# Optimization experiments

Hardware: AMD Instinct MI355X
Metric: run time of the kernel (lower is better)

## Reference

```python
import jax, jax.numpy as jnp
import numpy as np

B, L, DIM, HEADS = 4, 1024, 512, 8
HD = DIM // HEADS
HID = max(64, DIM // 2)
WIN = 32
SPARSITY = 0.3
TEMP = 1.0
PAT_TAU = 0.5


def setup_inputs() -> dict:
    key = jax.random.key(0)
    ks = jax.random.split(key, 8)
    gn = lambda k, shape, sc: jax.random.normal(k, shape, jnp.float32) * sc
    return {
        "x": jax.random.normal(ks[0], (B, L, DIM), jnp.float32),
        "mask": jnp.ones((B, L), jnp.int32),
        "Wqkv": gn(ks[1], (3 * DIM, DIM), 0.02),
        "Wproj": gn(ks[2], (DIM, DIM), 0.02),
        "bproj": jnp.zeros((DIM,), jnp.float32),
        "Wsel1": gn(ks[3], (HID, DIM), 0.05),
        "bsel1": jnp.zeros((HID,), jnp.float32),
        "Wsel2": gn(ks[4], (3, HID), 0.05),
        "bsel2": jnp.zeros((3,), jnp.float32),
        "log_pattern_tau": jnp.asarray(np.log(PAT_TAU), jnp.float32),
        "sparse_w": gn(ks[5], (HEADS,), 0.2),
        "sparse_b": jnp.zeros((HEADS,), jnp.float32),
    }


def reference(x, mask, Wqkv, Wproj, bproj, Wsel1, bsel1, Wsel2, bsel2,
              log_pattern_tau, sparse_w, sparse_b):
    Bq, Lq, D = x.shape
    scale = HD ** -0.5
    qkv = (x @ Wqkv.T).reshape(Bq, Lq, 3, HEADS, HD)
    q = jnp.transpose(qkv[:, :, 0], (0, 2, 1, 3))  # (B,H,L,hd)
    k = jnp.transpose(qkv[:, :, 1], (0, 2, 1, 3))
    v = jnp.transpose(qkv[:, :, 2], (0, 2, 1, 3))
    scores = jnp.einsum('bhid,bhjd->bhij', q, k) * scale  # (B,H,L,L)

    # pattern selector on mean-pooled features (eval: no gumbel, no dropout)
    pooled = x.mean(axis=1)
    logits = jax.nn.relu(pooled @ Wsel1.T + bsel1) @ Wsel2.T + bsel2  # (B,3)
    tau = jnp.clip(jnp.exp(log_pattern_tau), 1e-4, 10.0)
    pw = jax.nn.softmax(logits / tau, axis=-1)  # (B,3)

    half = WIN // 2
    ii = jnp.arange(Lq)[:, None]
    jj = jnp.arange(Lq)[None, :]
    local = ((jj >= ii - half) & (jj <= ii + half)).astype(jnp.float32)

    # learned sparse top-k mask per head via kth-value threshold
    kk = max(1, int(Lq * (1.0 - SPARSITY)))
    s = scores * sparse_w[None, :, None, None] + sparse_b[None, :, None, None]
    kth = jax.lax.top_k(s, kk)[0][..., -1:]
    smask = (s >= kth).astype(jnp.float32)  # (B,H,L,L)

    combined = (pw[:, 0, None, None, None] * local[None, None]
                + pw[:, 1, None, None, None]
                + pw[:, 2, None, None, None] * smask)
    neg = jnp.float32(-1e9)
    scores = jnp.where(combined > 0.05, scores, neg)
    scores = jnp.where(mask[:, None, None, :] == 0, neg, scores)

    # fallback: if a row is fully masked, unmask position 0
    all_masked = jnp.all(scores <= neg + 1e-6, axis=-1)  # (B,H,L)
    scores = scores.at[..., 0].set(jnp.where(all_masked, 0.0, scores[..., 0]))

    attn = jax.nn.softmax(scores / TEMP, axis=-1)
    out = jnp.einsum('bhij,bhjd->bhid', attn, v)
    out = jnp.transpose(out, (0, 2, 1, 3)).reshape(Bq, Lq, D)
    return out @ Wproj.T + bproj
```

## Files before the change

### kernel.cpp

```cpp
#include <hip/hip_runtime.h>
#include <math.h>

typedef __attribute__((ext_vector_type(8))) short short8;
typedef __attribute__((ext_vector_type(4))) float floatx4;

#define MFMA16(a, b, c) __builtin_amdgcn_mfma_f32_16x16x32_bf16(a, b, c, 0, 0, 0)


#define FRAG512(row, k) (((size_t)((row) >> 4)) * 8192 + (((k) >> 5) * 512) + \
                         ((((k) >> 3) & 3) * 128) + (((row) & 15) * 8) + ((k) & 7))
#define FRAGQK(row, e)  (((size_t)((row) >> 4)) * 1024 + (((e) >> 5) * 512) + \
                         ((((e) >> 3) & 3) * 128) + (((row) & 15) * 8) + ((e) & 7))

#define OFF_XB    ((size_t)0)
#define OFF_WQKV  ((size_t)4194304)
#define OFF_WPROJ ((size_t)5767168)
#define OFF_Q     ((size_t)6291456)
#define OFF_K     ((size_t)10485760)
#define OFF_VT    ((size_t)14680064)
#define OFF_AT    ((size_t)18874368)
#define OFF_PW    ((size_t)23068672)
#define OFF_PAR   ((size_t)23069696)
#define OFF_W1T   ((size_t)23595008)

__device__ __forceinline__ unsigned short f2bf(float f) {
    unsigned u = __float_as_uint(f);
    return (unsigned short)((u + 0x7fffu + ((u >> 16) & 1u)) >> 16);
}
__device__ __forceinline__ float bf2f(unsigned short s) {
    return __uint_as_float((unsigned)s << 16);
}
__device__ __forceinline__ void gl16(const void* g, void* l) {
    __builtin_amdgcn_global_load_lds(
        (const __attribute__((address_space(1))) unsigned*)g,
        (__attribute__((address_space(3))) unsigned*)l, 16, 0, 0);
}

__device__ __forceinline__ void frag_cvt_tile(const float* __restrict__ src,
                                              unsigned short* __restrict__ dst,
                                              const int t, const float sc)
{
    const int ln = t & 15, quad = (t >> 4) & 3, kh = t >> 6;
    #pragma unroll
    for (int i = 0; i < 4; ++i) {
        const int kb = kh + i * 4;
        const float* s = src + (size_t)ln * 512 + kb * 32 + quad * 8;
        float4 f0 = *(const float4*)s;
        float4 f1 = *(const float4*)(s + 4);
        unsigned short o[8] = { f2bf(f0.x * sc), f2bf(f0.y * sc), f2bf(f0.z * sc), f2bf(f0.w * sc),
                                f2bf(f1.x * sc), f2bf(f1.y * sc), f2bf(f1.z * sc), f2bf(f1.w * sc) };
        unsigned short* d = dst + kb * 512 + (size_t)(t & 63) * 8;
        *(ushort4*)d       = make_ushort4(o[0], o[1], o[2], o[3]);
        *(ushort4*)(d + 4) = make_ushort4(o[4], o[5], o[6], o[7]);
    }
}

__global__ __launch_bounds__(256)
void cvt_all(const float* __restrict__ x, const float* __restrict__ wqkv,
             const float* __restrict__ wproj, const float* __restrict__ W1,
             unsigned short* __restrict__ xb, unsigned short* __restrict__ oq,
             unsigned short* __restrict__ op, float* __restrict__ partial,
             float* __restrict__ w1t)
{
    const int bid = blockIdx.x, t = threadIdx.x;
    if (bid < 256) {
        const int b = bid >> 6, lb = bid & 63;
        const size_t base = ((size_t)b * 1024 + lb * 16) * 512;
        float s0 = 0.f, s1 = 0.f;
        #pragma unroll 4
        for (int l = 0; l < 16; ++l) {
            s0 += x[base + (size_t)l * 512 + t];
            s1 += x[base + (size_t)l * 512 + t + 256];
        }
        partial[((size_t)b * 64 + lb) * 512 + t] = s0;
        partial[((size_t)b * 64 + lb) * 512 + t + 256] = s1;
    } else if (bid < 512) {
        const int rt = bid - 256;
        frag_cvt_tile(x + (size_t)rt * 16 * 512, xb + (size_t)rt * 8192, t, 1.f);
    } else if (bid < 640) {
        const int tile = bid - 512;
        if (tile < 96)
            frag_cvt_tile(wqkv + (size_t)tile * 16 * 512, oq + (size_t)tile * 8192, t, 1.f);
        else
            frag_cvt_tile(wproj + (size_t)(tile - 96) * 16 * 512,
                          op + (size_t)(tile - 96) * 8192, t, 1.f);
    } else {
        __shared__ float tl[64][65];
        const int tile = bid - 640;
        const int tr = tile >> 3, tc = tile & 7;
        const int lr = t >> 6, lc = t & 63;
        #pragma unroll
        for (int p = 0; p < 16; ++p) {
            const int r = p * 4 + lr;
            tl[r][lc] = W1[(size_t)(tr * 64 + r) * 512 + tc * 64 + lc];
        }
        __syncthreads();
        #pragma unroll
        for (int p = 0; p < 16; ++p) {
            const int d = p * 4 + lr;
            w1t[(size_t)(tc * 64 + d) * 256 + tr * 64 + lc] = tl[lc][d];
        }
    }
}

__global__ __launch_bounds__(128)
void gemm_qkv_sel(const unsigned short* __restrict__ xb, const unsigned short* __restrict__ wb,
                  unsigned short* __restrict__ qo, unsigned short* __restrict__ ko,
                  unsigned short* __restrict__ vo,
                  const float* __restrict__ partial, const float* __restrict__ w1t,
                  const float* __restrict__ b1, const float* __restrict__ W2,
                  const float* __restrict__ b2, const float* __restrict__ ltau,
                  float* __restrict__ pwout)
{
    __shared__ __align__(16) unsigned short tile[2][64 * 72];
    const int bx = blockIdx.x, by = blockIdx.y;
    const int t = threadIdx.x;
    const int w = t >> 6, l64 = t & 63;

    if (by == 64) {
        if (bx >= 4) return;
        const int b = bx;
        float* pooled = (float*)&tile[0][0];
        float* hpart  = pooled + 512;
        float* h1s    = hpart + 512;
        float* lg     = h1s + 256;
        #pragma unroll
        for (int c = 0; c < 4; ++c) {
            const int col = t + c * 128;
            float s = 0.f;
            for (int p = 0; p < 64; ++p) s += partial[((size_t)b * 64 + p) * 512 + col];
            pooled[col] = s * (1.f / 1024.f);
        }
        __syncthreads();
        {
            float4 acc = make_float4(0.f, 0.f, 0.f, 0.f);
            const float* wt = w1t + (size_t)w * 256 * 256 + l64 * 4;
            for (int d = 0; d < 256; ++d) {
                const float pv = pooled[w * 256 + d];
                float4 wv = *(const float4*)(wt + (size_t)d * 256);
                acc.x += pv * wv.x; acc.y += pv * wv.y;
                acc.z += pv * wv.z; acc.w += pv * wv.w;
            }
            *(float4*)&hpart[w * 256 + l64 * 4] = acc;
        }
        __syncthreads();
        {
            #pragma unroll
            for (int c = 0; c < 2; ++c) {
                const int r = t + c * 128;
                h1s[r] = fmaxf(hpart[r] + hpart[256 + r] + b1[r], 0.f);
            }
        }
        __syncthreads();
        if (t < 3) {
            float s = b2[t];
            const float* w2 = W2 + t * 256;
            for (int i = 0; i < 256; ++i) s += w2[i] * h1s[i];
            float tauv = fminf(fmaxf(expf(ltau[0]), 1e-4f), 10.f);
            lg[t] = s / tauv;
        }
        __syncthreads();
        if (t == 0) {
            float m = fmaxf(lg[0], fmaxf(lg[1], lg[2]));
            float e0 = expf(lg[0] - m), e1 = expf(lg[1] - m), e2 = expf(lg[2] - m);
            float inv = 1.f / (e0 + e1 + e2);
            pwout[b * 3 + 0] = e0 * inv;
            pwout[b * 3 + 1] = e1 * inv;
            pwout[b * 3 + 2] = e2 * inv;
        }
        return;
    }

    const int ln = l64 & 15, quad = l64 >> 4;
    const int m0 = by << 6;
    const int nb0 = (bx << 7) + (w << 6);

    const unsigned short* Abase = xb + ((size_t)(m0 >> 4)) * 8192 + l64 * 8;
    const unsigned short* Bbase = wb + ((size_t)(nb0 >> 4)) * 8192 + l64 * 8;

    floatx4 acc[4][4];
    #pragma unroll
    for (int i = 0; i < 4; ++i)
        #pragma unroll
        for (int j = 0; j < 4; ++j) acc[i][j] = (floatx4){0.f, 0.f, 0.f, 0.f};

    short8 a0[4], b0[4], a1[4], b1v[4];
    #pragma unroll
    for (int i = 0; i < 4; ++i) {
        a0[i] = *(const short8*)(Abase + (size_t)i * 8192);
        b0[i] = *(const short8*)(Bbase + (size_t)i * 8192);
    }
    for (int s = 0; s < 16; s += 2) {
        #pragma unroll
        for (int i = 0; i < 4; ++i) {
            a1[i]  = *(const short8*)(Abase + (size_t)i * 8192 + (s + 1) * 512);
            b1v[i] = *(const short8*)(Bbase + (size_t)i * 8192 + (s + 1) * 512);
        }
        #pragma unroll
        for (int i = 0; i < 4; ++i)
            #pragma unroll
            for (int j = 0; j < 4; ++j)
                acc[i][j] = MFMA16(a0[i], b0[j], acc[i][j]);
        if (s + 2 < 16) {
            #pragma unroll
            for (int i = 0; i < 4; ++i) {
                a0[i] = *(const short8*)(Abase + (size_t)i * 8192 + (s + 2) * 512);
                b0[i] = *(const short8*)(Bbase + (size_t)i * 8192 + (s + 2) * 512);
            }
        }
        #pragma unroll
        for (int i = 0; i < 4; ++i)
            #pragma unroll
            for (int j = 0; j < 4; ++j)
                acc[i][j] = MFMA16(a1[i], b1v[j], acc[i][j]);
    }

    unsigned short* tw = &tile[w][0];
    const int which = bx >> 2;
    const int hh = (nb0 >> 6) & 7;
    const int g = (by >> 4) * 8 + hh;
    const int lrow0 = m0 & 1023;

    if (which == 2) {
        #pragma unroll
        for (int j = 0; j < 4; ++j)
            #pragma unroll
            for (int i = 0; i < 4; ++i)
                #pragma unroll
                for (int reg = 0; reg < 4; ++reg)
                    tw[(j * 16 + ln) * 72 + i * 16 + quad * 4 + reg] = f2bf(acc[i][j][reg]);
        const int chunk = lrow0 >> 7;
        const int ks0 = (lrow0 & 127) >> 5;
        unsigned short* dst = vo + (size_t)g * 65536 + (size_t)chunk * 8192;
        #pragma unroll
        for (int et = 0; et < 4; ++et)
            #pragma unroll
            for (int ksl = 0; ksl < 2; ++ksl) {
                const unsigned short* srcp = &tw[(et * 16 + ln) * 72 + ksl * 32 + quad * 8];
                *(short8*)(dst + (et * 4 + ks0 + ksl) * 512 + l64 * 8) = *(const short8*)srcp;
            }
    } else {
        const float sc = (which == 0) ? 0.125f : 1.f;
        #pragma unroll
        for (int j = 0; j < 4; ++j)
            #pragma unroll
            for (int i = 0; i < 4; ++i)
                #pragma unroll
                for (int reg = 0; reg < 4; ++reg)
                    tw[(i * 16 + quad * 4 + reg) * 72 + j * 16 + ln] = f2bf(acc[i][j][reg] * sc);
        unsigned short* dst = (which == 0 ? qo : ko) + (size_t)g * 65536;
        #pragma unroll
        for (int rt = 0; rt < 4; ++rt)
            #pragma unroll
            for (int eh = 0; eh < 2; ++eh) {
                const unsigned short* srcp = &tw[(rt * 16 + ln) * 72 + eh * 32 + quad * 8];
                *(short8*)(dst + ((size_t)((lrow0 >> 4) + rt)) * 1024 + eh * 512 + l64 * 8) =
                    *(const short8*)srcp;
            }
    }
}

__global__ __launch_bounds__(64)
void gemm_proj(const unsigned short* __restrict__ ab, const unsigned short* __restrict__ wb,
               const float* __restrict__ bias, float* __restrict__ out)
{
    const int t = threadIdx.x;
    const int ln = t & 15, quad = t >> 4;
    const int n0 = blockIdx.x << 6, m0 = blockIdx.y << 5;

    const unsigned short* Abase = ab + ((size_t)(m0 >> 4)) * 8192 + t * 8;
    const unsigned short* Bbase = wb + ((size_t)(n0 >> 4)) * 8192 + t * 8;

    floatx4 acc[2][4];
    #pragma unroll
    for (int i = 0; i < 2; ++i)
        #pragma unroll
        for (int j = 0; j < 4; ++j) acc[i][j] = (floatx4){0.f, 0.f, 0.f, 0.f};

    short8 a0[2], b0[4], a1[2], b1v[4];
    #pragma unroll
    for (int i = 0; i < 2; ++i) a0[i] = *(const short8*)(Abase + (size_t)i * 8192);
    #pragma unroll
    for (int j = 0; j < 4; ++j) b0[j] = *(const short8*)(Bbase + (size_t)j * 8192);
    for (int s = 0; s < 16; s += 2) {
        #pragma unroll
        for (int i = 0; i < 2; ++i) a1[i]  = *(const short8*)(Abase + (size_t)i * 8192 + (s + 1) * 512);
        #pragma unroll
        for (int j = 0; j < 4; ++j) b1v[j] = *(const short8*)(Bbase + (size_t)j * 8192 + (s + 1) * 512);
        #pragma unroll
        for (int i = 0; i < 2; ++i)
            #pragma unroll
            for (int j = 0; j < 4; ++j)
                acc[i][j] = MFMA16(a0[i], b0[j], acc[i][j]);
        if (s + 2 < 16) {
            #pragma unroll
            for (int i = 0; i < 2; ++i) a0[i] = *(const short8*)(Abase + (size_t)i * 8192 + (s + 2) * 512);
            #pragma unroll
            for (int j = 0; j < 4; ++j) b0[j] = *(const short8*)(Bbase + (size_t)j * 8192 + (s + 2) * 512);
        }
        #pragma unroll
        for (int i = 0; i < 2; ++i)
            #pragma unroll
            for (int j = 0; j < 4; ++j)
                acc[i][j] = MFMA16(a1[i], b1v[j], acc[i][j]);
    }
    #pragma unroll
    for (int j = 0; j < 4; ++j) {
        const float bv = bias[n0 + j * 16 + ln];
        #pragma unroll
        for (int i = 0; i < 2; ++i)
            #pragma unroll
            for (int reg = 0; reg < 4; ++reg)
                out[(size_t)(m0 + i * 16 + quad * 4 + reg) * 512 + n0 + j * 16 + ln] =
                    acc[i][j][reg] + bv;
    }
}

__global__ __launch_bounds__(256)
void attn_flash(const unsigned short* __restrict__ qm, const unsigned short* __restrict__ km,
                const unsigned short* __restrict__ vm, const int* __restrict__ mask,
                const float* __restrict__ pw, const float* __restrict__ sw,
                const float* __restrict__ sb, unsigned short* __restrict__ aout)
{
    __shared__ int mk[1024];
    __shared__ __align__(16) unsigned short Ks[8192];
    __shared__ __align__(16) unsigned short Vs[8192];
    __shared__ float PO[4][16][68];
    __shared__ unsigned kths[4][16];

    const int t = threadIdx.x;
    const int w = t >> 6, l64 = t & 63;
    const int ln = l64 & 15, quad = l64 >> 4;
    const int g = blockIdx.x & 31;
    const int rg = blockIdx.x >> 5;
    const int b = g >> 3, h = g & 7;
    const int i0 = rg * 64 + w * 16;

    const unsigned short* qg = qm + (size_t)g * 65536;
    const unsigned short* kg = km + (size_t)g * 65536;
    const unsigned short* vg = vm + (size_t)g * 65536;

    *(int4*)&mk[t * 4] = *(const int4*)(mask + b * 1024 + t * 4);

    const float pw0 = pw[b * 3 + 0], pw1 = pw[b * 3 + 1], pw2 = pw[b * 3 + 2];
    const bool a00 = pw1 > 0.05f;
    const bool a10 = (pw0 * 1.0f + pw1) > 0.05f;
    const bool a01 = (pw1 + pw2) > 0.05f;
    const bool a11 = ((pw0 * 1.0f + pw1) + pw2) > 0.05f;
    const bool need_sparse = (!a00 && a01) || (!a10 && a11);
    const bool flat_ok = (!need_sparse) && a00 && a10;
    const float w_h = sw[h], b_h = sb[h];
    __syncthreads();

    unsigned kth_r[4] = {0u, 0u, 0u, 0u};
    if (need_sparse) {
        unsigned* ub = (unsigned*)&PO[w][0][0];
        for (int r = 0; r < 16; ++r) {
            for (int c = 0; c < 16; ++c) {
                const int col = c * 64 + l64;
                float s = 0.f;
                for (int e = 0; e < 64; ++e)
                    s += bf2f(qg[FRAGQK(i0 + r, e)]) * bf2f(kg[FRAGQK(col, e)]);
                unsigned uu = __float_as_uint(s * w_h + b_h);
                ub[col] = (uu & 0x80000000u) ? ~uu : (uu | 0x80000000u);
            }
            unsigned u[16];
            #pragma unroll
            for (int c = 0; c < 16; ++c) u[c] = ub[l64 + c * 64];
            unsigned act = 0xFFFFu, p = 0u;
            int kk = 716;
            for (int bit = 31; bit >= 0; --bit) {
                unsigned ones = 0u;
                #pragma unroll
                for (int c = 0; c < 16; ++c)
                    if (((act >> c) & 1u) && ((u[c] >> bit) & 1u)) ones |= (1u << c);
                int c1 = __popc(ones);
                for (int off = 32; off; off >>= 1) c1 += __shfl_xor(c1, off);
                if (kk <= c1) { p |= (1u << bit); act &= ones; }
                else          { kk -= c1; act &= ~ones; }
            }
            if (l64 == 0) kths[w][r] = p;
        }
        #pragma unroll
        for (int reg = 0; reg < 4; ++reg) kth_r[reg] = kths[w][quad * 4 + reg];
    }

    const short8 aq0 = *(const short8*)(qg + ((size_t)(i0 >> 4)) * 1024 + l64 * 8);
    const short8 aq1 = *(const short8*)(qg + ((size_t)(i0 >> 4)) * 1024 + 512 + l64 * 8);

    float m_r[4] = {-3e38f, -3e38f, -3e38f, -3e38f};
    float l_r[4] = {0.f, 0.f, 0.f, 0.f};
    floatx4 accv[4];
    #pragma unroll
    for (int et = 0; et < 4; ++et) accv[et] = (floatx4){0.f, 0.f, 0.f, 0.f};
    unsigned short* Pw = (unsigned short*)&PO[w][0][0];

    for (int jc = 0; jc < 8; ++jc) {
        const int j0 = jc << 7;
        {
            const unsigned short* kc = kg + (size_t)j0 * 64;
            const unsigned short* vc = vg + ((size_t)(j0 >> 7)) * 8192;
            #pragma unroll
            for (int c = 0; c < 4; ++c) {
                const int bi = w * 4 + c;
                gl16(kc + bi * 512 + l64 * 8, (char*)Ks + bi * 1024);
                gl16(vc + bi * 512 + l64 * 8, (char*)Vs + bi * 1024);
            }
        }
        const bool mall = __all((mk[j0 + l64] != 0) && (mk[j0 + 64 + l64] != 0));
        const bool fast = flat_ok && mall;
        __syncthreads();

        floatx4 sfr[8];
        #pragma unroll
        for (int nt = 0; nt < 8; ++nt) {
            const short8 kb0 = *(const short8*)(Ks + nt * 1024 + l64 * 8);
            const short8 kb1 = *(const short8*)(Ks + nt * 1024 + 512 + l64 * 8);
            floatx4 z = (floatx4){0.f, 0.f, 0.f, 0.f};
            z = MFMA16(aq0, kb0, z);
            z = MFMA16(aq1, kb1, z);
            sfr[nt] = z;
        }

        float rm[4] = {-3e38f, -3e38f, -3e38f, -3e38f};
        if (fast) {
            #pragma unroll
            for (int nt = 0; nt < 8; ++nt)
                #pragma unroll
                for (int reg = 0; reg < 4; ++reg) rm[reg] = fmaxf(rm[reg], sfr[nt][reg]);
        } else {
            #pragma unroll
            for (int nt = 0; nt < 8; ++nt) {
                const int j = j0 + nt * 16 + ln;
                const bool mk0 = (mk[j] == 0);
                #pragma unroll
                for (int reg = 0; reg < 4; ++reg) {
                    const int i = i0 + quad * 4 + reg;
                    const float s = sfr[nt][reg];
                    const bool loc = (j >= i - 16) && (j <= i + 16);
                    bool sm = false;
                    if (need_sparse) {
                        unsigned uu = __float_as_uint(s * w_h + b_h);
                        unsigned key = (uu & 0x80000000u) ? ~uu : (uu | 0x80000000u);
                        sm = key >= kth_r[reg];
                    }
                    bool allowed = loc ? (sm ? a11 : a10) : (sm ? a01 : a00);
                    if (mk0) allowed = false;
                    const float se = allowed ? s : -1e9f;
                    sfr[nt][reg] = se;
                    rm[reg] = fmaxf(rm[reg], se);
                }
            }
        }
        #pragma unroll
        for (int reg = 0; reg < 4; ++reg) {
            float v = rm[reg];
            v = fmaxf(v, __shfl_xor(v, 1));
            v = fmaxf(v, __shfl_xor(v, 2));
            v = fmaxf(v, __shfl_xor(v, 4));
            v = fmaxf(v, __shfl_xor(v, 8));
            rm[reg] = v;
        }
        float alpha[4], rs[4];
        #pragma unroll
        for (int reg = 0; reg < 4; ++reg) {
            const float mn = fmaxf(m_r[reg], rm[reg]);
            alpha[reg] = __expf(m_r[reg] - mn);
            m_r[reg] = mn;
            rs[reg] = 0.f;
        }
        #pragma unroll
        for (int nt = 0; nt < 8; ++nt)
            #pragma unroll
            for (int reg = 0; reg < 4; ++reg) {
                const float p = __expf(sfr[nt][reg] - m_r[reg]);
                rs[reg] += p;
                Pw[(quad * 4 + reg) * 136 + nt * 16 + ln] = f2bf(p);
            }
        #pragma unroll
        for (int reg = 0; reg < 4; ++reg) {
            float v = rs[reg];
            v += __shfl_xor(v, 1);
            v += __shfl_xor(v, 2);
            v += __shfl_xor(v, 4);
            v += __shfl_xor(v, 8);
            l_r[reg] = l_r[reg] * alpha[reg] + v;
        }
        short8 pa[4];
        #pragma unroll
        for (int ks = 0; ks < 4; ++ks)
            pa[ks] = *(const short8*)&Pw[ln * 136 + ks * 32 + quad * 8];
        #pragma unroll
        for (int et = 0; et < 4; ++et) {
            floatx4 a = accv[et];
            a[0] *= alpha[0]; a[1] *= alpha[1]; a[2] *= alpha[2]; a[3] *= alpha[3];
            #pragma unroll
            for (int ks = 0; ks < 4; ++ks) {
                const short8 bv = *(const short8*)(Vs + (et * 4 + ks) * 512 + l64 * 8);
                a = MFMA16(pa[ks], bv, a);
            }
            accv[et] = a;
        }
        __syncthreads();
    }

    #pragma unroll
    for (int et = 0; et < 4; ++et)
        #pragma unroll
        for (int reg = 0; reg < 4; ++reg) {
            float val;
            if (m_r[reg] <= -1e9f + 1e-6f)
                val = bf2f(vg[et * 2048 + ln * 8]);
            else
                val = accv[et][reg] / l_r[reg];
            PO[w][quad * 4 + reg][et * 16 + ln] = val;
        }
    #pragma unroll
    for (int rr = 0; rr < 4; ++rr) {
        const int r = (l64 >> 4) * 4 + rr;
        const int cb = (l64 & 15) * 4;
        float4 ov = *(const float4*)&PO[w][r][cb];
        ushort4 res = make_ushort4(f2bf(ov.x), f2bf(ov.y), f2bf(ov.z), f2bf(ov.w));
        const int row_g = b * 1024 + i0 + r;
        const int col = h * 64 + cb;
        *(ushort4*)&aout[FRAG512(row_g, col)] = res;
    }
}

extern "C" void kernel_launch(void* const* d_in, const int* in_sizes, int n_in,
                              void* d_out, int out_size, void* d_ws, size_t ws_size,
                              hipStream_t stream) {
    const float* x     = (const float*)d_in[0];
    const int*   mask  = (const int*)d_in[1];
    const float* Wqkv  = (const float*)d_in[2];
    const float* Wproj = (const float*)d_in[3];
    const float* bproj = (const float*)d_in[4];
    const float* Wsel1 = (const float*)d_in[5];
    const float* bsel1 = (const float*)d_in[6];
    const float* Wsel2 = (const float*)d_in[7];
    const float* bsel2 = (const float*)d_in[8];
    const float* ltau  = (const float*)d_in[9];
    const float* sw    = (const float*)d_in[10];
    const float* sb    = (const float*)d_in[11];
    char* ws = (char*)d_ws;
    unsigned short* xb     = (unsigned short*)(ws + OFF_XB);
    unsigned short* wqkvb  = (unsigned short*)(ws + OFF_WQKV);
    unsigned short* wprojb = (unsigned short*)(ws + OFF_WPROJ);
    unsigned short* q      = (unsigned short*)(ws + OFF_Q);
    unsigned short* k      = (unsigned short*)(ws + OFF_K);
    unsigned short* v      = (unsigned short*)(ws + OFF_VT);
    unsigned short* attnb  = (unsigned short*)(ws + OFF_AT);
    float* pw  = (float*)(ws + OFF_PW);
    float* par = (float*)(ws + OFF_PAR);
    float* w1t = (float*)(ws + OFF_W1T);
    float* out = (float*)d_out;
    (void)in_sizes; (void)n_in; (void)out_size; (void)ws_size;

    cvt_all<<<672, 256, 0, stream>>>(x, Wqkv, Wproj, Wsel1, xb, wqkvb, wprojb, par, w1t);
    gemm_qkv_sel<<<dim3(12, 65), 128, 0, stream>>>(xb, wqkvb, q, k, v,
                                                   par, w1t, bsel1, Wsel2, bsel2, ltau, pw);
    attn_flash<<<512, 256, 0, stream>>>(q, k, v, mask, pw, sw, sb, attnb);
    gemm_proj<<<dim3(8, 128), 64, 0, stream>>>(attnb, wprojb, bproj, out);
}
```

Measured before the change: 151.8 us.

## Split attention over key halves with a separate merge kernel, register V loads

Attention now runs as a split-KV kernel: each block handles half of the key range, writing unnormalized partial outputs plus row max and sum to workspace, and a new merge kernel combines the two halves and writes bf16 output. This doubles the block count to raise occupancy, and V is loaded straight into registers with a software prefetch instead of going through LDS. Separately, the conversion kernel fuses the x mean-pool partial sums with x bf16 conversion, dropping 256 blocks. Costs are an extra launch and fp32 partial traffic. The top-k threshold pass is now repeated in both halves.

Result: slower. 158.9 us (+4.7%).

```diff
diff --git a/kernel.cpp b/kernel.cpp
--- a/kernel.cpp
+++ b/kernel.cpp
@@ -22,6 +22,9 @@
 #define OFF_PW    ((size_t)23068672)
 #define OFF_PAR   ((size_t)23069696)
 #define OFF_W1T   ((size_t)23595008)
+#define OFF_PO    ((size_t)24119296)
+#define OFF_PM    ((size_t)40896512)
+#define OFF_PL    ((size_t)41158656)
 
 __device__ __forceinline__ unsigned short f2bf(float f) {
     unsigned u = __float_as_uint(f);
@@ -64,21 +67,19 @@
 {
     const int bid = blockIdx.x, t = threadIdx.x;
     if (bid < 256) {
-        const int b = bid >> 6, lb = bid & 63;
-        const size_t base = ((size_t)b * 1024 + lb * 16) * 512;
+        const int rt = bid;
+        const float* src = x + (size_t)rt * 16 * 512;
+        frag_cvt_tile(src, xb + (size_t)rt * 8192, t, 1.f);
         float s0 = 0.f, s1 = 0.f;
         #pragma unroll 4
         for (int l = 0; l < 16; ++l) {
-            s0 += x[base + (size_t)l * 512 + t];
-            s1 += x[base + (size_t)l * 512 + t + 256];
-        }
-        partial[((size_t)b * 64 + lb) * 512 + t] = s0;
-        partial[((size_t)b * 64 + lb) * 512 + t + 256] = s1;
-    } else if (bid < 512) {
-        const int rt = bid - 256;
-        frag_cvt_tile(x + (size_t)rt * 16 * 512, xb + (size_t)rt * 8192, t, 1.f);
-    } else if (bid < 640) {
-        const int tile = bid - 512;
+            s0 += src[(size_t)l * 512 + t];
+            s1 += src[(size_t)l * 512 + t + 256];
+        }
+        partial[(size_t)rt * 512 + t] = s0;
+        partial[(size_t)rt * 512 + t + 256] = s1;
+    } else if (bid < 384) {
+        const int tile = bid - 256;
         if (tile < 96)
             frag_cvt_tile(wqkv + (size_t)tile * 16 * 512, oq + (size_t)tile * 8192, t, 1.f);
         else
@@ -86,7 +87,7 @@
                           op + (size_t)(tile - 96) * 8192, t, 1.f);
     } else {
         __shared__ float tl[64][65];
-        const int tile = bid - 640;
+        const int tile = bid - 384;
         const int tr = tile >> 3, tc = tile & 7;
         const int lr = t >> 6, lc = t & 63;
         #pragma unroll
@@ -317,30 +318,33 @@
 }
 
 __global__ __launch_bounds__(256)
-void attn_flash(const unsigned short* __restrict__ qm, const unsigned short* __restrict__ km,
-                const unsigned short* __restrict__ vm, const int* __restrict__ mask,
-                const float* __restrict__ pw, const float* __restrict__ sw,
-                const float* __restrict__ sb, unsigned short* __restrict__ aout)
+void attn_part(const unsigned short* __restrict__ qm, const unsigned short* __restrict__ km,
+               const unsigned short* __restrict__ vm, const int* __restrict__ mask,
+               const float* __restrict__ pw, const float* __restrict__ sw,
+               const float* __restrict__ sb,
+               float* __restrict__ Op, float* __restrict__ Pm, float* __restrict__ Pl)
 {
-    __shared__ int mk[1024];
+    __shared__ int mk[512];
     __shared__ __align__(16) unsigned short Ks[8192];
-    __shared__ __align__(16) unsigned short Vs[8192];
     __shared__ float PO[4][16][68];
     __shared__ unsigned kths[4][16];
 
     const int t = threadIdx.x;
     const int w = t >> 6, l64 = t & 63;
     const int ln = l64 & 15, quad = l64 >> 4;
-    const int g = blockIdx.x & 31;
-    const int rg = blockIdx.x >> 5;
+    const int bid = blockIdx.x;
+    const int g = bid & 31;
+    const int rt = (bid >> 5) & 15;
+    const int half = bid >> 9;
     const int b = g >> 3, h = g & 7;
-    const int i0 = rg * 64 + w * 16;
+    const int i0 = rt * 64 + w * 16;
+    const int j0base = half * 512;
 
     const unsigned short* qg = qm + (size_t)g * 65536;
     const unsigned short* kg = km + (size_t)g * 65536;
     const unsigned short* vg = vm + (size_t)g * 65536;
 
-    *(int4*)&mk[t * 4] = *(const int4*)(mask + b * 1024 + t * 4);
+    *(int2*)&mk[t * 2] = *(const int2*)(mask + b * 1024 + j0base + t * 2);
 
     const float pw0 = pw[b * 3 + 0], pw1 = pw[b * 3 + 1], pw2 = pw[b * 3 + 2];
     const bool a00 = pw1 > 0.05f;
@@ -383,6 +387,7 @@
         }
         #pragma unroll
         for (int reg = 0; reg < 4; ++reg) kth_r[reg] = kths[w][quad * 4 + reg];
+        __syncthreads();
     }
 
     const short8 aq0 = *(const short8*)(qg + ((size_t)(i0 >> 4)) * 1024 + l64 * 8);
@@ -395,19 +400,25 @@
     for (int et = 0; et < 4; ++et) accv[et] = (floatx4){0.f, 0.f, 0.f, 0.f};
     unsigned short* Pw = (unsigned short*)&PO[w][0][0];
 
-    for (int jc = 0; jc < 8; ++jc) {
-        const int j0 = jc << 7;
+    for (int jc = 0; jc < 4; ++jc) {
+        const int jcg = half * 4 + jc;
+        const int j0 = jcg << 7;
+        const int jl0 = jc << 7;
+        if (jc) __syncthreads();
         {
-            const unsigned short* kc = kg + (size_t)j0 * 64;
-            const unsigned short* vc = vg + ((size_t)(j0 >> 7)) * 8192;
+            const unsigned short* kc = kg + (size_t)jcg * 8192;
             #pragma unroll
             for (int c = 0; c < 4; ++c) {
                 const int bi = w * 4 + c;
                 gl16(kc + bi * 512 + l64 * 8, (char*)Ks + bi * 1024);
-                gl16(vc + bi * 512 + l64 * 8, (char*)Vs + bi * 1024);
-            }
-        }
-        const bool mall = __all((mk[j0 + l64] != 0) && (mk[j0 + 64 + l64] != 0));
+            }
+        }
+        const unsigned short* vbase = vg + (size_t)jcg * 8192 + l64 * 8;
+        short8 vb_cur[4], vb_nxt[4];
+        #pragma unroll
+        for (int ks = 0; ks < 4; ++ks)
+            vb_cur[ks] = *(const short8*)(vbase + ks * 512);
+        const bool mall = __all((mk[jl0 + l64] != 0) && (mk[jl0 + 64 + l64] != 0));
         const bool fast = flat_ok && mall;
         __syncthreads();
 
@@ -432,7 +443,7 @@
             #pragma unroll
             for (int nt = 0; nt < 8; ++nt) {
                 const int j = j0 + nt * 16 + ln;
-                const bool mk0 = (mk[j] == 0);
+                const bool mk0 = (mk[j - j0base] == 0);
                 #pragma unroll
                 for (int reg = 0; reg < 4; ++reg) {
                     const int i = i0 + quad * 4 + reg;
@@ -492,38 +503,90 @@
             pa[ks] = *(const short8*)&Pw[ln * 136 + ks * 32 + quad * 8];
         #pragma unroll
         for (int et = 0; et < 4; ++et) {
+            if (et < 3) {
+                #pragma unroll
+                for (int ks = 0; ks < 4; ++ks)
+                    vb_nxt[ks] = *(const short8*)(vbase + ((et + 1) * 4 + ks) * 512);
+            }
             floatx4 a = accv[et];
             a[0] *= alpha[0]; a[1] *= alpha[1]; a[2] *= alpha[2]; a[3] *= alpha[3];
             #pragma unroll
-            for (int ks = 0; ks < 4; ++ks) {
-                const short8 bv = *(const short8*)(Vs + (et * 4 + ks) * 512 + l64 * 8);
-                a = MFMA16(pa[ks], bv, a);
-            }
+            for (int ks = 0; ks < 4; ++ks) a = MFMA16(pa[ks], vb_cur[ks], a);
             accv[et] = a;
-        }
-        __syncthreads();
+            #pragma unroll
+            for (int ks = 0; ks < 4; ++ks) vb_cur[ks] = vb_nxt[ks];
+        }
     }
 
     #pragma unroll
     for (int et = 0; et < 4; ++et)
         #pragma unroll
+        for (int reg = 0; reg < 4; ++reg)
+            PO[w][quad * 4 + reg][et * 16 + ln] = accv[et][reg];
+    if (ln == 0) {
+        #pragma unroll
         for (int reg = 0; reg < 4; ++reg) {
-            float val;
-            if (m_r[reg] <= -1e9f + 1e-6f)
-                val = bf2f(vg[et * 2048 + ln * 8]);
-            else
-                val = accv[et][reg] / l_r[reg];
-            PO[w][quad * 4 + reg][et * 16 + ln] = val;
-        }
+            const int row = w * 16 + quad * 4 + reg;
+            Pm[(size_t)bid * 64 + row] = m_r[reg];
+            Pl[(size_t)bid * 64 + row] = l_r[reg];
+        }
+    }
+    float* dstO = Op + ((size_t)bid * 64 + w * 16) * 64;
     #pragma unroll
     for (int rr = 0; rr < 4; ++rr) {
         const int r = (l64 >> 4) * 4 + rr;
         const int cb = (l64 & 15) * 4;
         float4 ov = *(const float4*)&PO[w][r][cb];
-        ushort4 res = make_ushort4(f2bf(ov.x), f2bf(ov.y), f2bf(ov.z), f2bf(ov.w));
-        const int row_g = b * 1024 + i0 + r;
-        const int col = h * 64 + cb;
-        *(ushort4*)&aout[FRAG512(row_g, col)] = res;
+        *(float4*)(dstO + (size_t)r * 64 + cb) = ov;
+    }
+}
+
+__global__ __launch_bounds__(256)
+void attn_merge(const float* __restrict__ Op, const float* __restrict__ Pm,
+                const float* __restrict__ Pl, const unsigned short* __restrict__ vm,
+                unsigned short* __restrict__ aout)
+{
+    const int p = blockIdx.x;
+    const int g = p & 31, rt = p >> 5;
+    const int b = g >> 3, h = g & 7;
+    const int t = threadIdx.x;
+    const int r = t >> 2, eo = (t & 3) * 16;
+    const int b0 = p, b1 = p + 512;
+
+    const float m0 = Pm[(size_t)b0 * 64 + r], m1 = Pm[(size_t)b1 * 64 + r];
+    const float l0 = Pl[(size_t)b0 * 64 + r], l1 = Pl[(size_t)b1 * 64 + r];
+    const float M = fmaxf(m0, m1);
+    const unsigned short* vg = vm + (size_t)g * 65536;
+    const int row_g = b * 1024 + rt * 64 + r;
+
+    if (M <= -1e9f + 1e-6f) {
+        #pragma unroll
+        for (int e4 = 0; e4 < 4; ++e4) {
+            const int e = eo + e4 * 4;
+            ushort4 res;
+            res.x = vg[((e + 0) >> 4) * 2048 + ((e + 0) & 15) * 8];
+            res.y = vg[((e + 1) >> 4) * 2048 + ((e + 1) & 15) * 8];
+            res.z = vg[((e + 2) >> 4) * 2048 + ((e + 2) & 15) * 8];
+            res.w = vg[((e + 3) >> 4) * 2048 + ((e + 3) & 15) * 8];
+            *(ushort4*)&aout[FRAG512(row_g, h * 64 + e)] = res;
+        }
+        return;
+    }
+    const float s0 = __expf(m0 - M), s1 = __expf(m1 - M);
+    const float L = l0 * s0 + l1 * s1;
+    const float inv = 1.f / L;
+    const float* o0 = Op + ((size_t)b0 * 64 + r) * 64 + eo;
+    const float* o1 = Op + ((size_t)b1 * 64 + r) * 64 + eo;
+    #pragma unroll
+    for (int e4 = 0; e4 < 4; ++e4) {
+        float4 a = *(const float4*)(o0 + e4 * 4);
+        float4 c = *(const float4*)(o1 + e4 * 4);
+        ushort4 res;
+        res.x = f2bf((a.x * s0 + c.x * s1) * inv);
+        res.y = f2bf((a.y * s0 + c.y * s1) * inv);
+        res.z = f2bf((a.z * s0 + c.z * s1) * inv);
+        res.w = f2bf((a.w * s0 + c.w * s1) * inv);
+        *(ushort4*)&aout[FRAG512(row_g, h * 64 + eo + e4 * 4)] = res;
     }
 }
 
@@ -553,12 +616,16 @@
     float* pw  = (float*)(ws + OFF_PW);
     float* par = (float*)(ws + OFF_PAR);
     float* w1t = (float*)(ws + OFF_W1T);
+    float* Op  = (float*)(ws + OFF_PO);
+    float* Pm  = (float*)(ws + OFF_PM);
+    float* Pl  = (float*)(ws + OFF_PL);
     float* out = (float*)d_out;
     (void)in_sizes; (void)n_in; (void)out_size; (void)ws_size;
 
-    cvt_all<<<672, 256, 0, stream>>>(x, Wqkv, Wproj, Wsel1, xb, wqkvb, wprojb, par, w1t);
+    cvt_all<<<416, 256, 0, stream>>>(x, Wqkv, Wproj, Wsel1, xb, wqkvb, wprojb, par, w1t);
     gemm_qkv_sel<<<dim3(12, 65), 128, 0, stream>>>(xb, wqkvb, q, k, v,
                                                    par, w1t, bsel1, Wsel2, bsel2, ltau, pw);
-    attn_flash<<<512, 256, 0, stream>>>(q, k, v, mask, pw, sw, sb, attnb);
+    attn_part<<<1024, 256, 0, stream>>>(q, k, v, mask, pw, sw, sb, Op, Pm, Pl);
+    attn_merge<<<512, 256, 0, stream>>>(Op, Pm, Pl, v, attnb);
     gemm_proj<<<dim3(8, 128), 64, 0, stream>>>(attnb, wprojb, bproj, out);
 }
```
